# Performance work log

Measured on AMD Instinct MI355X. Metric: run time of the kernel, lower is better.

Reference implementation:

```python
import jax, jax.numpy as jnp
import numpy as np

N, C_S, C_Z, H, D = 512, 384, 128, 16, 24  # c_hidden per head
EPS = 1e-5

def _ln(x, g, b):
    m = jnp.mean(x, axis=-1, keepdims=True)
    v = jnp.mean(jnp.square(x - m), axis=-1, keepdims=True)
    return (x - m) * jax.lax.rsqrt(v + EPS) * g + b

def setup_inputs() -> dict:
    key = jax.random.key(0)
    ks = jax.random.split(key, 12)
    s = lambda fan: 1.0 / np.sqrt(fan)
    return {
        "a": jax.random.normal(ks[0], (1, N, C_S), jnp.float32),
        "z": jax.random.normal(ks[1], (1, N, N, C_Z), jnp.float32),
        "g_a": jnp.ones((C_S,), jnp.float32),
        "b_a": jnp.zeros((C_S,), jnp.float32),
        "g_z": jnp.ones((C_Z,), jnp.float32),
        "b_z": jnp.zeros((C_Z,), jnp.float32),
        "Wz": jax.random.normal(ks[2], (C_Z, H), jnp.float32) * s(C_Z),
        "bz": jnp.zeros((H,), jnp.float32),
        "Wq": jax.random.normal(ks[3], (C_S, H * D), jnp.float32) * s(C_S),
        "Wk": jax.random.normal(ks[4], (C_S, H * D), jnp.float32) * s(C_S),
        "Wv": jax.random.normal(ks[5], (C_S, H * D), jnp.float32) * s(C_S),
        "Wg": jax.random.normal(ks[6], (C_S, H * D), jnp.float32) * s(C_S),
        "bg": jnp.zeros((H * D,), jnp.float32),
        "Wo": jax.random.normal(ks[7], (H * D, C_S), jnp.float32) * s(H * D),
        "bo": jnp.zeros((C_S,), jnp.float32),
    }

def reference(a, z, g_a, b_a, g_z, b_z, Wz, bz, Wq, Wk, Wv, Wg, bg, Wo, bo):
    B = a.shape[0]
    a_n = _ln(a, g_a, b_a)                       # [B,N,C_S]
    z_n = _ln(z, g_z, b_z)                       # [B,N,N,C_Z]
    # linear_z then permute(0,3,1,2): [B,N,N,H] -> [B,H,N,N]
    pair_bias = jnp.einsum('bijc,ch->bhij', z_n, Wz) + bz[None, :, None, None]
    q = (a_n @ Wq).reshape(B, N, H, D) * (1.0 / np.sqrt(D))
    k = (a_n @ Wk).reshape(B, N, H, D)
    v = (a_n @ Wv).reshape(B, N, H, D)
    scores = jnp.einsum('bqhd,bkhd->bhqk', q, k) + pair_bias
    p = jax.nn.softmax(scores, axis=-1)
    o = jnp.einsum('bhqk,bkhd->bqhd', p, v)      # [B,N,H,D]
    g = jax.nn.sigmoid(a_n @ Wg + bg).reshape(B, N, H, D)
    o = (o * g).reshape(B, N, H * D)
    return o @ Wo + bo                            # [B,N,C_S]
```

## Files before the change

kernel.cpp:

```cpp
#include <hip/hip_runtime.h>
#include <math.h>

#define N 512
#define CS 384
#define CZ 128
#define NH 16
#define DH 24
#define HD 384
#define NN (N*N)
#define EPS 1e-5f

#define OFF_AN   0
#define OFF_QT   196608
#define OFF_KT   393216
#define OFF_VT   589824
#define OFF_GT   786432
#define OFF_OG   983040
#define OFF_WZ2  1179648
#define OFF_SH   1181696
#define OFF_BH   1181712
#define OFF_BIAS 1181728

__global__ void prep_kernel(const float* __restrict__ g_z, const float* __restrict__ lnb_z,
                            const float* __restrict__ Wz, const float* __restrict__ bz,
                            float* __restrict__ wz2, float* __restrict__ sh, float* __restrict__ bh) {
    int t = threadIdx.x;
    for (int i = t; i < NH * CZ; i += 256) {
        int h = i >> 7, c = i & (CZ - 1);
        wz2[h * CZ + c] = g_z[c] * Wz[c * NH + h];
    }
    __shared__ float ls[NH][17], lb[NH][17];
    int h = t >> 4, seg = t & 15;
    float s = 0.f, b = 0.f;
    #pragma unroll
    for (int i = 0; i < 8; ++i) {
        int c = seg * 8 + i;
        float w = Wz[c * NH + h];
        s += g_z[c] * w;
        b += lnb_z[c] * w;
    }
    ls[h][seg] = s; lb[h][seg] = b;
    __syncthreads();
    if (t < NH) {
        float ss = 0.f, bb = 0.f;
        #pragma unroll
        for (int i = 0; i < 16; ++i) { ss += ls[t][i]; bb += lb[t][i]; }
        sh[t] = ss;
        bh[t] = bb + bz[t];
    }
}

__global__ void ln_a_kernel(const float* __restrict__ a, const float* __restrict__ g_a,
                            const float* __restrict__ b_a, float* __restrict__ an_out) {
    int r = blockIdx.x, t = threadIdx.x;
    const float* row = a + r * CS;
    float x0 = row[t], x1 = row[t + 128], x2 = row[t + 256];
    float s1 = x0 + x1 + x2;
    float s2 = x0 * x0 + x1 * x1 + x2 * x2;
    #pragma unroll
    for (int m = 1; m < 64; m <<= 1) {
        s1 += __shfl_xor(s1, m, 64);
        s2 += __shfl_xor(s2, m, 64);
    }
    __shared__ float ls1[2], ls2[2];
    if ((t & 63) == 0) { ls1[t >> 6] = s1; ls2[t >> 6] = s2; }
    __syncthreads();
    s1 = ls1[0] + ls1[1];
    s2 = ls2[0] + ls2[1];
    float mu = s1 * (1.f / CS);
    float var = s2 * (1.f / CS) - mu * mu;
    float rs = rsqrtf(var + EPS);
    float* an = an_out + r * CS;
    an[t]       = (x0 - mu) * rs * g_a[t]       + b_a[t];
    an[t + 128] = (x1 - mu) * rs * g_a[t + 128] + b_a[t + 128];
    an[t + 256] = (x2 - mu) * rs * g_a[t + 256] + b_a[t + 256];
}

__global__ void __launch_bounds__(256) qkvg_kernel(const float* __restrict__ Wq, const float* __restrict__ Wk,
                                                   const float* __restrict__ Wv, const float* __restrict__ Wg,
                                                   const float* __restrict__ bg, const float* __restrict__ an,
                                                   float* __restrict__ qt, float* __restrict__ kt,
                                                   float* __restrict__ vt, float* __restrict__ gt) {
    const int lane = threadIdx.x & 63;
    const int w = __builtin_amdgcn_readfirstlane(threadIdx.x >> 6);
    const int strip = blockIdx.x * 4 + w;
    const int n0 = strip * 8;
    const int sel = n0 / HD;
    const int col = n0 % HD;
    const float* Wm = (sel == 0) ? Wq : (sel == 1) ? Wk : (sel == 2) ? Wv : Wg;
    const int m = blockIdx.y * 64 + lane;
    const float* arow = an + m * CS;
    float acc[8];
    #pragma unroll
    for (int j = 0; j < 8; ++j) acc[j] = 0.f;
    for (int kb = 0; kb < CS; kb += 32) {
        float4 av[8];
        #pragma unroll
        for (int i = 0; i < 8; ++i) av[i] = ((const float4*)(arow + kb))[i];
        #pragma unroll
        for (int i = 0; i < 8; ++i) {
            const float* wr = Wm + (kb + i * 4) * HD + col;
            #pragma unroll
            for (int j = 0; j < 8; ++j) {
                acc[j] += av[i].x * wr[j];
                acc[j] += av[i].y * wr[HD + j];
                acc[j] += av[i].z * wr[2 * HD + j];
                acc[j] += av[i].w * wr[3 * HD + j];
            }
        }
    }
    float* dst = (sel == 0) ? qt : (sel == 1) ? kt : (sel == 2) ? vt : gt;
    if (sel == 3) {
        #pragma unroll
        for (int j = 0; j < 8; ++j) acc[j] = 1.f / (1.f + __expf(-(acc[j] + bg[col + j])));
    } else if (sel == 0) {
        #pragma unroll
        for (int j = 0; j < 8; ++j) acc[j] *= 0.20412414523193153f;
    }
    #pragma unroll
    for (int j = 0; j < 8; ++j) {
        int c = col + j;
        int h = c / DH, d = c % DH;
        dst[(h * N + m) * DH + d] = acc[j];
    }
}

__global__ void __launch_bounds__(256) pairbias_kernel(const float* __restrict__ z,
                                                       const float* __restrict__ wz2,
                                                       const float* __restrict__ sh,
                                                       const float* __restrict__ bh,
                                                       float* __restrict__ bias) {
    const int row = blockIdx.x * 256 + threadIdx.x;
    const float* zr = z + (size_t)row * CZ;
    float dots[NH];
    #pragma unroll
    for (int h = 0; h < NH; ++h) dots[h] = 0.f;
    float s1 = 0.f, s2 = 0.f;
    #pragma unroll
    for (int cb = 0; cb < CZ; cb += 32) {
        float4 zv[8];
        #pragma unroll
        for (int i = 0; i < 8; ++i) zv[i] = ((const float4*)(zr + cb))[i];
        #pragma unroll
        for (int i = 0; i < 8; ++i) {
            s1 += zv[i].x + zv[i].y + zv[i].z + zv[i].w;
            s2 += zv[i].x * zv[i].x + zv[i].y * zv[i].y + zv[i].z * zv[i].z + zv[i].w * zv[i].w;
        }
        #pragma unroll
        for (int h = 0; h < NH; ++h) {
            const float* wrow = wz2 + h * CZ + cb;
            float d = dots[h];
            #pragma unroll
            for (int i = 0; i < 8; ++i) {
                d += zv[i].x * wrow[i * 4 + 0];
                d += zv[i].y * wrow[i * 4 + 1];
                d += zv[i].z * wrow[i * 4 + 2];
                d += zv[i].w * wrow[i * 4 + 3];
            }
            dots[h] = d;
        }
    }
    float mu = s1 * (1.f / CZ);
    float var = s2 * (1.f / CZ) - mu * mu;
    float r = rsqrtf(var + EPS);
    #pragma unroll
    for (int h = 0; h < NH; ++h)
        bias[h * NN + row] = r * (dots[h] - mu * sh[h]) + bh[h];
}

__global__ void __launch_bounds__(256) attn_kernel(const float* __restrict__ qt, const float* __restrict__ kt,
                                                   const float* __restrict__ vt, const float* __restrict__ gt,
                                                   const float* __restrict__ bias, float* __restrict__ og) {
    const int lane = threadIdx.x & 63;
    const int w = __builtin_amdgcn_readfirstlane(threadIdx.x >> 6);
    const int qhalf = lane >> 5;
    const int klane = lane & 31;
    const int h = blockIdx.y;
    const int q = blockIdx.x * 8 + w * 2 + qhalf;
    const float* qT = qt + h * N * DH;
    const float* kT = kt + h * N * DH;
    const float* vT = vt + h * N * DH;

    float qv[DH];
    #pragma unroll
    for (int d6 = 0; d6 < 6; ++d6) {
        float4 t4 = ((const float4*)(qT + q * DH))[d6];
        qv[d6 * 4 + 0] = t4.x; qv[d6 * 4 + 1] = t4.y; qv[d6 * 4 + 2] = t4.z; qv[d6 * 4 + 3] = t4.w;
    }
    float sc[16];
    #pragma unroll
    for (int t = 0; t < 16; ++t) {
        const int kk = t * 32 + klane;
        const float4* kr = (const float4*)(kT + kk * DH);
        float4 k0 = kr[0], k1 = kr[1], k2 = kr[2], k3 = kr[3], k4 = kr[4], k5 = kr[5];
        float s = qv[0]*k0.x + qv[1]*k0.y + qv[2]*k0.z + qv[3]*k0.w
                + qv[4]*k1.x + qv[5]*k1.y + qv[6]*k1.z + qv[7]*k1.w
                + qv[8]*k2.x + qv[9]*k2.y + qv[10]*k2.z + qv[11]*k2.w
                + qv[12]*k3.x + qv[13]*k3.y + qv[14]*k3.z + qv[15]*k3.w
                + qv[16]*k4.x + qv[17]*k4.y + qv[18]*k4.z + qv[19]*k4.w
                + qv[20]*k5.x + qv[21]*k5.y + qv[22]*k5.z + qv[23]*k5.w;
        sc[t] = s + bias[h * NN + q * N + kk];
    }
    float mx = sc[0];
    #pragma unroll
    for (int t = 1; t < 16; ++t) mx = fmaxf(mx, sc[t]);
    #pragma unroll
    for (int m = 1; m < 32; m <<= 1) mx = fmaxf(mx, __shfl_xor(mx, m, 64));
    float sum = 0.f;
    #pragma unroll
    for (int t = 0; t < 16; ++t) { sc[t] = __expf(sc[t] - mx); sum += sc[t]; }
    #pragma unroll
    for (int m = 1; m < 32; m <<= 1) sum += __shfl_xor(sum, m, 64);
    float inv = 1.f / sum;
    #pragma unroll
    for (int t = 0; t < 16; ++t) sc[t] *= inv;
    float acc[DH];
    #pragma unroll
    for (int d = 0; d < DH; ++d) acc[d] = 0.f;
    #pragma unroll
    for (int t = 0; t < 16; ++t) {
        const int kk = t * 32 + klane;
        const float4* vr = (const float4*)(vT + kk * DH);
        float4 v0 = vr[0], v1 = vr[1], v2 = vr[2], v3 = vr[3], v4 = vr[4], v5 = vr[5];
        float p = sc[t];
        acc[0] += p*v0.x;  acc[1] += p*v0.y;  acc[2] += p*v0.z;  acc[3] += p*v0.w;
        acc[4] += p*v1.x;  acc[5] += p*v1.y;  acc[6] += p*v1.z;  acc[7] += p*v1.w;
        acc[8] += p*v2.x;  acc[9] += p*v2.y;  acc[10] += p*v2.z; acc[11] += p*v2.w;
        acc[12] += p*v3.x; acc[13] += p*v3.y; acc[14] += p*v3.z; acc[15] += p*v3.w;
        acc[16] += p*v4.x; acc[17] += p*v4.y; acc[18] += p*v4.z; acc[19] += p*v4.w;
        acc[20] += p*v5.x; acc[21] += p*v5.y; acc[22] += p*v5.z; acc[23] += p*v5.w;
    }
    #pragma unroll
    for (int m = 1; m < 32; m <<= 1) {
        #pragma unroll
        for (int d = 0; d < DH; ++d) acc[d] += __shfl_xor(acc[d], m, 64);
    }
    float o = 0.f;
    #pragma unroll
    for (int d = 0; d < DH; ++d) o = (klane == d) ? acc[d] : o;
    if (klane < DH) {
        float g = gt[h * N * DH + q * DH + klane];
        og[q * HD + h * DH + klane] = o * g;
    }
}

__global__ void __launch_bounds__(256) out_gemm_kernel(const float* __restrict__ Wo, const float* __restrict__ bo,
                                                       const float* __restrict__ og, float* __restrict__ out) {
    const int lane = threadIdx.x & 63;
    const int w = __builtin_amdgcn_readfirstlane(threadIdx.x >> 6);
    const int strip = blockIdx.x * 4 + w;
    const int c0 = strip * 4;
    const int m = blockIdx.y * 64 + lane;
    const float* orow = og + m * HD;
    float acc[4];
    #pragma unroll
    for (int j = 0; j < 4; ++j) acc[j] = 0.f;
    for (int kb = 0; kb < HD; kb += 32) {
        float4 av[8];
        #pragma unroll
        for (int i = 0; i < 8; ++i) av[i] = ((const float4*)(orow + kb))[i];
        #pragma unroll
        for (int i = 0; i < 8; ++i) {
            const float* wr = Wo + (kb + i * 4) * CS + c0;
            #pragma unroll
            for (int j = 0; j < 4; ++j) {
                acc[j] += av[i].x * wr[j];
                acc[j] += av[i].y * wr[CS + j];
                acc[j] += av[i].z * wr[2 * CS + j];
                acc[j] += av[i].w * wr[3 * CS + j];
            }
        }
    }
    #pragma unroll
    for (int j = 0; j < 4; ++j) out[m * CS + c0 + j] = acc[j] + bo[c0 + j];
}

extern "C" void kernel_launch(void* const* d_in, const int* in_sizes, int n_in,
                              void* d_out, int out_size, void* d_ws, size_t ws_size,
                              hipStream_t stream) {
    const float* a    = (const float*)d_in[0];
    const float* z    = (const float*)d_in[1];
    const float* g_a  = (const float*)d_in[2];
    const float* b_a  = (const float*)d_in[3];
    const float* g_z  = (const float*)d_in[4];
    const float* b_z  = (const float*)d_in[5];
    const float* Wz   = (const float*)d_in[6];
    const float* bz   = (const float*)d_in[7];
    const float* Wq   = (const float*)d_in[8];
    const float* Wk   = (const float*)d_in[9];
    const float* Wv   = (const float*)d_in[10];
    const float* Wg   = (const float*)d_in[11];
    const float* bg   = (const float*)d_in[12];
    const float* Wo   = (const float*)d_in[13];
    const float* bo   = (const float*)d_in[14];
    float* ws  = (float*)d_ws;
    float* out = (float*)d_out;

    float* an   = ws + OFF_AN;
    float* qt   = ws + OFF_QT;
    float* kt   = ws + OFF_KT;
    float* vt   = ws + OFF_VT;
    float* gt   = ws + OFF_GT;
    float* ogp  = ws + OFF_OG;
    float* wz2  = ws + OFF_WZ2;
    float* shp  = ws + OFF_SH;
    float* bhp  = ws + OFF_BH;
    float* bias = ws + OFF_BIAS;

    hipLaunchKernelGGL(prep_kernel,     dim3(1),      dim3(256), 0, stream, g_z, b_z, Wz, bz, wz2, shp, bhp);
    hipLaunchKernelGGL(ln_a_kernel,     dim3(512),    dim3(128), 0, stream, a, g_a, b_a, an);
    hipLaunchKernelGGL(qkvg_kernel,     dim3(48, 8),  dim3(256), 0, stream, Wq, Wk, Wv, Wg, bg, an, qt, kt, vt, gt);
    hipLaunchKernelGGL(pairbias_kernel, dim3(1024),   dim3(256), 0, stream, z, wz2, shp, bhp, bias);
    hipLaunchKernelGGL(attn_kernel,     dim3(64, 16), dim3(256), 0, stream, qt, kt, vt, gt, bias, ogp);
    hipLaunchKernelGGL(out_gemm_kernel, dim3(24, 8),  dim3(256), 0, stream, Wo, bo, ogp, out);
}
```

Measured before the change: 338.5 us.

## Merge prep/LN and QKVG/pair-bias kernels, narrow GEMM strips for more waves

Result: slower. 362.8 us (+7.2%).

```diff
diff --git a/kernel.cpp b/kernel.cpp
--- a/kernel.cpp
+++ b/kernel.cpp
@@ -21,40 +21,45 @@
 #define OFF_BH   1181712
 #define OFF_BIAS 1181728
 
-__global__ void prep_kernel(const float* __restrict__ g_z, const float* __restrict__ lnb_z,
-                            const float* __restrict__ Wz, const float* __restrict__ bz,
-                            float* __restrict__ wz2, float* __restrict__ sh, float* __restrict__ bh) {
-    int t = threadIdx.x;
-    for (int i = t; i < NH * CZ; i += 256) {
-        int h = i >> 7, c = i & (CZ - 1);
-        wz2[h * CZ + c] = g_z[c] * Wz[c * NH + h];
-    }
+__global__ void __launch_bounds__(256) ln_prep_kernel(const float* __restrict__ a, const float* __restrict__ g_a,
+                                                      const float* __restrict__ b_a, float* __restrict__ an_out,
+                                                      const float* __restrict__ g_z, const float* __restrict__ lnb_z,
+                                                      const float* __restrict__ Wz, const float* __restrict__ bz,
+                                                      float* __restrict__ wz2, float* __restrict__ sh,
+                                                      float* __restrict__ bh) {
     __shared__ float ls[NH][17], lb[NH][17];
-    int h = t >> 4, seg = t & 15;
-    float s = 0.f, b = 0.f;
-    #pragma unroll
-    for (int i = 0; i < 8; ++i) {
-        int c = seg * 8 + i;
-        float w = Wz[c * NH + h];
-        s += g_z[c] * w;
-        b += lnb_z[c] * w;
-    }
-    ls[h][seg] = s; lb[h][seg] = b;
-    __syncthreads();
-    if (t < NH) {
-        float ss = 0.f, bb = 0.f;
-        #pragma unroll
-        for (int i = 0; i < 16; ++i) { ss += ls[t][i]; bb += lb[t][i]; }
-        sh[t] = ss;
-        bh[t] = bb + bz[t];
-    }
-}
-
-__global__ void ln_a_kernel(const float* __restrict__ a, const float* __restrict__ g_a,
-                            const float* __restrict__ b_a, float* __restrict__ an_out) {
-    int r = blockIdx.x, t = threadIdx.x;
+    __shared__ float l1[4], l2[4];
+    const int t = threadIdx.x;
+    if (blockIdx.x == 256) {
+        for (int i = t; i < NH * CZ; i += 256) {
+            int h = i >> 7, c = i & (CZ - 1);
+            wz2[h * CZ + c] = g_z[c] * Wz[c * NH + h];
+        }
+        int h = t >> 4, seg = t & 15;
+        float s = 0.f, b = 0.f;
+        #pragma unroll
+        for (int i = 0; i < 8; ++i) {
+            int c = seg * 8 + i;
+            float w = Wz[c * NH + h];
+            s += g_z[c] * w;
+            b += lnb_z[c] * w;
+        }
+        ls[h][seg] = s; lb[h][seg] = b;
+        __syncthreads();
+        if (t < NH) {
+            float ss = 0.f, bb = 0.f;
+            #pragma unroll
+            for (int i = 0; i < 16; ++i) { ss += ls[t][i]; bb += lb[t][i]; }
+            sh[t] = ss;
+            bh[t] = bb + bz[t];
+        }
+        return;
+    }
+    const int half = t >> 7;
+    const int tr = t & 127;
+    const int r = blockIdx.x * 2 + half;
     const float* row = a + r * CS;
-    float x0 = row[t], x1 = row[t + 128], x2 = row[t + 256];
+    float x0 = row[tr], x1 = row[tr + 128], x2 = row[tr + 256];
     float s1 = x0 + x1 + x2;
     float s2 = x0 * x0 + x1 * x1 + x2 * x2;
     #pragma unroll
@@ -62,110 +67,111 @@
         s1 += __shfl_xor(s1, m, 64);
         s2 += __shfl_xor(s2, m, 64);
     }
-    __shared__ float ls1[2], ls2[2];
-    if ((t & 63) == 0) { ls1[t >> 6] = s1; ls2[t >> 6] = s2; }
+    if ((t & 63) == 0) { l1[t >> 6] = s1; l2[t >> 6] = s2; }
     __syncthreads();
-    s1 = ls1[0] + ls1[1];
-    s2 = ls2[0] + ls2[1];
+    s1 = l1[half * 2] + l1[half * 2 + 1];
+    s2 = l2[half * 2] + l2[half * 2 + 1];
     float mu = s1 * (1.f / CS);
     float var = s2 * (1.f / CS) - mu * mu;
     float rs = rsqrtf(var + EPS);
     float* an = an_out + r * CS;
-    an[t]       = (x0 - mu) * rs * g_a[t]       + b_a[t];
-    an[t + 128] = (x1 - mu) * rs * g_a[t + 128] + b_a[t + 128];
-    an[t + 256] = (x2 - mu) * rs * g_a[t + 256] + b_a[t + 256];
-}
-
-__global__ void __launch_bounds__(256) qkvg_kernel(const float* __restrict__ Wq, const float* __restrict__ Wk,
-                                                   const float* __restrict__ Wv, const float* __restrict__ Wg,
-                                                   const float* __restrict__ bg, const float* __restrict__ an,
-                                                   float* __restrict__ qt, float* __restrict__ kt,
-                                                   float* __restrict__ vt, float* __restrict__ gt) {
-    const int lane = threadIdx.x & 63;
-    const int w = __builtin_amdgcn_readfirstlane(threadIdx.x >> 6);
-    const int strip = blockIdx.x * 4 + w;
-    const int n0 = strip * 8;
-    const int sel = n0 / HD;
-    const int col = n0 % HD;
-    const float* Wm = (sel == 0) ? Wq : (sel == 1) ? Wk : (sel == 2) ? Wv : Wg;
-    const int m = blockIdx.y * 64 + lane;
-    const float* arow = an + m * CS;
-    float acc[8];
-    #pragma unroll
-    for (int j = 0; j < 8; ++j) acc[j] = 0.f;
-    for (int kb = 0; kb < CS; kb += 32) {
-        float4 av[8];
-        #pragma unroll
-        for (int i = 0; i < 8; ++i) av[i] = ((const float4*)(arow + kb))[i];
-        #pragma unroll
-        for (int i = 0; i < 8; ++i) {
-            const float* wr = Wm + (kb + i * 4) * HD + col;
-            #pragma unroll
-            for (int j = 0; j < 8; ++j) {
-                acc[j] += av[i].x * wr[j];
-                acc[j] += av[i].y * wr[HD + j];
-                acc[j] += av[i].z * wr[2 * HD + j];
-                acc[j] += av[i].w * wr[3 * HD + j];
+    an[tr]       = (x0 - mu) * rs * g_a[tr]       + b_a[tr];
+    an[tr + 128] = (x1 - mu) * rs * g_a[tr + 128] + b_a[tr + 128];
+    an[tr + 256] = (x2 - mu) * rs * g_a[tr + 256] + b_a[tr + 256];
+}
+
+__global__ void __launch_bounds__(256) qp_kernel(const float* __restrict__ Wq, const float* __restrict__ Wk,
+                                                 const float* __restrict__ Wv, const float* __restrict__ Wg,
+                                                 const float* __restrict__ bg, const float* __restrict__ an,
+                                                 float* __restrict__ qt, float* __restrict__ kt,
+                                                 float* __restrict__ vt, float* __restrict__ gt,
+                                                 const float* __restrict__ z, const float* __restrict__ wz2,
+                                                 const float* __restrict__ sh, const float* __restrict__ bh,
+                                                 float* __restrict__ bias) {
+    const int b = blockIdx.x;
+    if (b < 768) {
+        const int lane = threadIdx.x & 63;
+        const int w = __builtin_amdgcn_readfirstlane(threadIdx.x >> 6);
+        const int wid = b * 4 + w;
+        const int strip = wid >> 3;
+        const int mb = wid & 7;
+        const int n0 = strip * 4;
+        const int sel = n0 / HD;
+        const int col = n0 % HD;
+        const float* Wm = (sel == 0) ? Wq : (sel == 1) ? Wk : (sel == 2) ? Wv : Wg;
+        const int m = mb * 64 + lane;
+        const float* arow = an + m * CS;
+        float acc[4];
+        #pragma unroll
+        for (int j = 0; j < 4; ++j) acc[j] = 0.f;
+        for (int kb = 0; kb < CS; kb += 32) {
+            float4 av[8];
+            #pragma unroll
+            for (int i = 0; i < 8; ++i) av[i] = ((const float4*)(arow + kb))[i];
+            #pragma unroll
+            for (int i = 0; i < 8; ++i) {
+                const float* wr = Wm + (kb + i * 4) * HD + col;
+                #pragma unroll
+                for (int j = 0; j < 4; ++j) {
+                    acc[j] += av[i].x * wr[j];
+                    acc[j] += av[i].y * wr[HD + j];
+                    acc[j] += av[i].z * wr[2 * HD + j];
+                    acc[j] += av[i].w * wr[3 * HD + j];
+                }
             }
         }
-    }
-    float* dst = (sel == 0) ? qt : (sel == 1) ? kt : (sel == 2) ? vt : gt;
-    if (sel == 3) {
-        #pragma unroll
-        for (int j = 0; j < 8; ++j) acc[j] = 1.f / (1.f + __expf(-(acc[j] + bg[col + j])));
-    } else if (sel == 0) {
-        #pragma unroll
-        for (int j = 0; j < 8; ++j) acc[j] *= 0.20412414523193153f;
-    }
-    #pragma unroll
-    for (int j = 0; j < 8; ++j) {
-        int c = col + j;
-        int h = c / DH, d = c % DH;
-        dst[(h * N + m) * DH + d] = acc[j];
-    }
-}
-
-__global__ void __launch_bounds__(256) pairbias_kernel(const float* __restrict__ z,
-                                                       const float* __restrict__ wz2,
-                                                       const float* __restrict__ sh,
-                                                       const float* __restrict__ bh,
-                                                       float* __restrict__ bias) {
-    const int row = blockIdx.x * 256 + threadIdx.x;
-    const float* zr = z + (size_t)row * CZ;
-    float dots[NH];
-    #pragma unroll
-    for (int h = 0; h < NH; ++h) dots[h] = 0.f;
-    float s1 = 0.f, s2 = 0.f;
-    #pragma unroll
-    for (int cb = 0; cb < CZ; cb += 32) {
-        float4 zv[8];
-        #pragma unroll
-        for (int i = 0; i < 8; ++i) zv[i] = ((const float4*)(zr + cb))[i];
-        #pragma unroll
-        for (int i = 0; i < 8; ++i) {
-            s1 += zv[i].x + zv[i].y + zv[i].z + zv[i].w;
-            s2 += zv[i].x * zv[i].x + zv[i].y * zv[i].y + zv[i].z * zv[i].z + zv[i].w * zv[i].w;
-        }
-        #pragma unroll
-        for (int h = 0; h < NH; ++h) {
-            const float* wrow = wz2 + h * CZ + cb;
-            float d = dots[h];
+        float* dst = (sel == 0) ? qt : (sel == 1) ? kt : (sel == 2) ? vt : gt;
+        if (sel == 3) {
+            #pragma unroll
+            for (int j = 0; j < 4; ++j) acc[j] = 1.f / (1.f + __expf(-(acc[j] + bg[col + j])));
+        } else if (sel == 0) {
+            #pragma unroll
+            for (int j = 0; j < 4; ++j) acc[j] *= 0.20412414523193153f;
+        }
+        #pragma unroll
+        for (int j = 0; j < 4; ++j) {
+            int c = col + j;
+            int h = c / DH, d = c % DH;
+            dst[(h * N + m) * DH + d] = acc[j];
+        }
+    } else {
+        const int row = (b - 768) * 256 + threadIdx.x;
+        const float* zr = z + (size_t)row * CZ;
+        float dots[NH];
+        #pragma unroll
+        for (int h = 0; h < NH; ++h) dots[h] = 0.f;
+        float s1 = 0.f, s2 = 0.f;
+        #pragma unroll
+        for (int cb = 0; cb < CZ; cb += 32) {
+            float4 zv[8];
+            #pragma unroll
+            for (int i = 0; i < 8; ++i) zv[i] = ((const float4*)(zr + cb))[i];
             #pragma unroll
             for (int i = 0; i < 8; ++i) {
-                d += zv[i].x * wrow[i * 4 + 0];
-                d += zv[i].y * wrow[i * 4 + 1];
-                d += zv[i].z * wrow[i * 4 + 2];
-                d += zv[i].w * wrow[i * 4 + 3];
+                s1 += zv[i].x + zv[i].y + zv[i].z + zv[i].w;
+                s2 += zv[i].x * zv[i].x + zv[i].y * zv[i].y + zv[i].z * zv[i].z + zv[i].w * zv[i].w;
             }
-            dots[h] = d;
-        }
-    }
-    float mu = s1 * (1.f / CZ);
-    float var = s2 * (1.f / CZ) - mu * mu;
-    float r = rsqrtf(var + EPS);
-    #pragma unroll
-    for (int h = 0; h < NH; ++h)
-        bias[h * NN + row] = r * (dots[h] - mu * sh[h]) + bh[h];
+            #pragma unroll
+            for (int h = 0; h < NH; ++h) {
+                const float* wrow = wz2 + h * CZ + cb;
+                float d = dots[h];
+                #pragma unroll
+                for (int i = 0; i < 8; ++i) {
+                    d += zv[i].x * wrow[i * 4 + 0];
+                    d += zv[i].y * wrow[i * 4 + 1];
+                    d += zv[i].z * wrow[i * 4 + 2];
+                    d += zv[i].w * wrow[i * 4 + 3];
+                }
+                dots[h] = d;
+            }
+        }
+        float mu = s1 * (1.f / CZ);
+        float var = s2 * (1.f / CZ) - mu * mu;
+        float r = rsqrtf(var + EPS);
+        #pragma unroll
+        for (int h = 0; h < NH; ++h)
+            bias[h * NN + row] = r * (dots[h] - mu * sh[h]) + bh[h];
+    }
 }
 
 __global__ void __launch_bounds__(256) attn_kernel(const float* __restrict__ qt, const float* __restrict__ kt,
@@ -248,13 +254,14 @@
                                                        const float* __restrict__ og, float* __restrict__ out) {
     const int lane = threadIdx.x & 63;
     const int w = __builtin_amdgcn_readfirstlane(threadIdx.x >> 6);
-    const int strip = blockIdx.x * 4 + w;
-    const int c0 = strip * 4;
-    const int m = blockIdx.y * 64 + lane;
+    const int wid = blockIdx.x * 4 + w;
+    const int strip = wid >> 3;
+    const int mb = wid & 7;
+    const int c0 = strip * 2;
+    const int m = mb * 64 + lane;
     const float* orow = og + m * HD;
-    float acc[4];
-    #pragma unroll
-    for (int j = 0; j < 4; ++j) acc[j] = 0.f;
+    float acc[2];
+    acc[0] = 0.f; acc[1] = 0.f;
     for (int kb = 0; kb < HD; kb += 32) {
         float4 av[8];
         #pragma unroll
@@ -263,7 +270,7 @@
         for (int i = 0; i < 8; ++i) {
             const float* wr = Wo + (kb + i * 4) * CS + c0;
             #pragma unroll
-            for (int j = 0; j < 4; ++j) {
+            for (int j = 0; j < 2; ++j) {
                 acc[j] += av[i].x * wr[j];
                 acc[j] += av[i].y * wr[CS + j];
                 acc[j] += av[i].z * wr[2 * CS + j];
@@ -272,7 +279,7 @@
         }
     }
     #pragma unroll
-    for (int j = 0; j < 4; ++j) out[m * CS + c0 + j] = acc[j] + bo[c0 + j];
+    for (int j = 0; j < 2; ++j) out[m * CS + c0 + j] = acc[j] + bo[c0 + j];
 }
 
 extern "C" void kernel_launch(void* const* d_in, const int* in_sizes, int n_in,
@@ -307,10 +314,12 @@
     float* bhp  = ws + OFF_BH;
     float* bias = ws + OFF_BIAS;
 
-    hipLaunchKernelGGL(prep_kernel,     dim3(1),      dim3(256), 0, stream, g_z, b_z, Wz, bz, wz2, shp, bhp);
-    hipLaunchKernelGGL(ln_a_kernel,     dim3(512),    dim3(128), 0, stream, a, g_a, b_a, an);
-    hipLaunchKernelGGL(qkvg_kernel,     dim3(48, 8),  dim3(256), 0, stream, Wq, Wk, Wv, Wg, bg, an, qt, kt, vt, gt);
-    hipLaunchKernelGGL(pairbias_kernel, dim3(1024),   dim3(256), 0, stream, z, wz2, shp, bhp, bias);
-    hipLaunchKernelGGL(attn_kernel,     dim3(64, 16), dim3(256), 0, stream, qt, kt, vt, gt, bias, ogp);
-    hipLaunchKernelGGL(out_gemm_kernel, dim3(24, 8),  dim3(256), 0, stream, Wo, bo, ogp, out);
-}
+    hipLaunchKernelGGL(ln_prep_kernel, dim3(257),    dim3(256), 0, stream,
+                       a, g_a, b_a, an, g_z, b_z, Wz, bz, wz2, shp, bhp);
+    hipLaunchKernelGGL(qp_kernel,      dim3(1792),   dim3(256), 0, stream,
+                       Wq, Wk, Wv, Wg, bg, an, qt, kt, vt, gt, z, wz2, shp, bhp, bias);
+    hipLaunchKernelGGL(attn_kernel,    dim3(64, 16), dim3(256), 0, stream,
+                       qt, kt, vt, gt, bias, ogp);
+    hipLaunchKernelGGL(out_gemm_kernel, dim3(384),   dim3(256), 0, stream,
+                       Wo, bo, ogp, out);
+}
```

## Split pair-bias rows across 16 lanes with shuffle reductions; merge LN and prep kernels

Applied to the files above, without the earlier changes.

Result: slower. 356.4 us (+5.3%).

```diff
diff --git a/kernel.cpp b/kernel.cpp
--- a/kernel.cpp
+++ b/kernel.cpp
@@ -21,40 +21,45 @@
 #define OFF_BH   1181712
 #define OFF_BIAS 1181728
 
-__global__ void prep_kernel(const float* __restrict__ g_z, const float* __restrict__ lnb_z,
-                            const float* __restrict__ Wz, const float* __restrict__ bz,
-                            float* __restrict__ wz2, float* __restrict__ sh, float* __restrict__ bh) {
-    int t = threadIdx.x;
-    for (int i = t; i < NH * CZ; i += 256) {
-        int h = i >> 7, c = i & (CZ - 1);
-        wz2[h * CZ + c] = g_z[c] * Wz[c * NH + h];
-    }
+__global__ void __launch_bounds__(256) ln_prep_kernel(const float* __restrict__ a, const float* __restrict__ g_a,
+                                                      const float* __restrict__ b_a, float* __restrict__ an_out,
+                                                      const float* __restrict__ g_z, const float* __restrict__ lnb_z,
+                                                      const float* __restrict__ Wz, const float* __restrict__ bz,
+                                                      float* __restrict__ wz2, float* __restrict__ sh,
+                                                      float* __restrict__ bh) {
     __shared__ float ls[NH][17], lb[NH][17];
-    int h = t >> 4, seg = t & 15;
-    float s = 0.f, b = 0.f;
-    #pragma unroll
-    for (int i = 0; i < 8; ++i) {
-        int c = seg * 8 + i;
-        float w = Wz[c * NH + h];
-        s += g_z[c] * w;
-        b += lnb_z[c] * w;
-    }
-    ls[h][seg] = s; lb[h][seg] = b;
-    __syncthreads();
-    if (t < NH) {
-        float ss = 0.f, bb = 0.f;
-        #pragma unroll
-        for (int i = 0; i < 16; ++i) { ss += ls[t][i]; bb += lb[t][i]; }
-        sh[t] = ss;
-        bh[t] = bb + bz[t];
-    }
-}
-
-__global__ void ln_a_kernel(const float* __restrict__ a, const float* __restrict__ g_a,
-                            const float* __restrict__ b_a, float* __restrict__ an_out) {
-    int r = blockIdx.x, t = threadIdx.x;
+    __shared__ float l1[4], l2[4];
+    const int t = threadIdx.x;
+    if (blockIdx.x == 256) {
+        for (int i = t; i < NH * CZ; i += 256) {
+            int h = i >> 7, c = i & (CZ - 1);
+            wz2[h * CZ + c] = g_z[c] * Wz[c * NH + h];
+        }
+        int h = t >> 4, seg = t & 15;
+        float s = 0.f, b = 0.f;
+        #pragma unroll
+        for (int i = 0; i < 8; ++i) {
+            int c = seg * 8 + i;
+            float w = Wz[c * NH + h];
+            s += g_z[c] * w;
+            b += lnb_z[c] * w;
+        }
+        ls[h][seg] = s; lb[h][seg] = b;
+        __syncthreads();
+        if (t < NH) {
+            float ss = 0.f, bb = 0.f;
+            #pragma unroll
+            for (int i = 0; i < 16; ++i) { ss += ls[t][i]; bb += lb[t][i]; }
+            sh[t] = ss;
+            bh[t] = bb + bz[t];
+        }
+        return;
+    }
+    const int half = t >> 7;
+    const int tr = t & 127;
+    const int r = blockIdx.x * 2 + half;
     const float* row = a + r * CS;
-    float x0 = row[t], x1 = row[t + 128], x2 = row[t + 256];
+    float x0 = row[tr], x1 = row[tr + 128], x2 = row[tr + 256];
     float s1 = x0 + x1 + x2;
     float s2 = x0 * x0 + x1 * x1 + x2 * x2;
     #pragma unroll
@@ -62,18 +67,17 @@
         s1 += __shfl_xor(s1, m, 64);
         s2 += __shfl_xor(s2, m, 64);
     }
-    __shared__ float ls1[2], ls2[2];
-    if ((t & 63) == 0) { ls1[t >> 6] = s1; ls2[t >> 6] = s2; }
+    if ((t & 63) == 0) { l1[t >> 6] = s1; l2[t >> 6] = s2; }
     __syncthreads();
-    s1 = ls1[0] + ls1[1];
-    s2 = ls2[0] + ls2[1];
+    s1 = l1[half * 2] + l1[half * 2 + 1];
+    s2 = l2[half * 2] + l2[half * 2 + 1];
     float mu = s1 * (1.f / CS);
     float var = s2 * (1.f / CS) - mu * mu;
     float rs = rsqrtf(var + EPS);
     float* an = an_out + r * CS;
-    an[t]       = (x0 - mu) * rs * g_a[t]       + b_a[t];
-    an[t + 128] = (x1 - mu) * rs * g_a[t + 128] + b_a[t + 128];
-    an[t + 256] = (x2 - mu) * rs * g_a[t + 256] + b_a[t + 256];
+    an[tr]       = (x0 - mu) * rs * g_a[tr]       + b_a[tr];
+    an[tr + 128] = (x1 - mu) * rs * g_a[tr + 128] + b_a[tr + 128];
+    an[tr + 256] = (x2 - mu) * rs * g_a[tr + 256] + b_a[tr + 256];
 }
 
 __global__ void __launch_bounds__(256) qkvg_kernel(const float* __restrict__ Wq, const float* __restrict__ Wk,
@@ -130,42 +134,44 @@
                                                        const float* __restrict__ sh,
                                                        const float* __restrict__ bh,
                                                        float* __restrict__ bias) {
-    const int row = blockIdx.x * 256 + threadIdx.x;
-    const float* zr = z + (size_t)row * CZ;
-    float dots[NH];
-    #pragma unroll
-    for (int h = 0; h < NH; ++h) dots[h] = 0.f;
-    float s1 = 0.f, s2 = 0.f;
-    #pragma unroll
-    for (int cb = 0; cb < CZ; cb += 32) {
-        float4 zv[8];
-        #pragma unroll
-        for (int i = 0; i < 8; ++i) zv[i] = ((const float4*)(zr + cb))[i];
-        #pragma unroll
-        for (int i = 0; i < 8; ++i) {
-            s1 += zv[i].x + zv[i].y + zv[i].z + zv[i].w;
-            s2 += zv[i].x * zv[i].x + zv[i].y * zv[i].y + zv[i].z * zv[i].z + zv[i].w * zv[i].w;
-        }
+    const int lane = threadIdx.x & 63;
+    const int w = threadIdx.x >> 6;
+    const int r4 = lane >> 4;
+    const int cl = lane & 15;
+    const int wave_row0 = blockIdx.x * 128 + w * 32;
+    const float shc = sh[cl];
+    const float bhc = bh[cl];
+    for (int g = 0; g < 8; ++g) {
+        const int row = wave_row0 + g * 4 + r4;
+        const float* zr = z + (size_t)row * CZ + cl * 8;
+        float4 z0 = ((const float4*)zr)[0];
+        float4 z1 = ((const float4*)zr)[1];
+        float s1 = z0.x + z0.y + z0.z + z0.w + z1.x + z1.y + z1.z + z1.w;
+        float s2 = z0.x*z0.x + z0.y*z0.y + z0.z*z0.z + z0.w*z0.w
+                 + z1.x*z1.x + z1.y*z1.y + z1.z*z1.z + z1.w*z1.w;
+        float dots[NH];
         #pragma unroll
         for (int h = 0; h < NH; ++h) {
-            const float* wrow = wz2 + h * CZ + cb;
-            float d = dots[h];
+            const float4* wp = (const float4*)(wz2 + h * CZ + cl * 8);
+            float4 w0 = wp[0], w1 = wp[1];
+            dots[h] = z0.x*w0.x + z0.y*w0.y + z0.z*w0.z + z0.w*w0.w
+                    + z1.x*w1.x + z1.y*w1.y + z1.z*w1.z + z1.w*w1.w;
+        }
+        #pragma unroll
+        for (int m = 1; m < 16; m <<= 1) {
+            s1 += __shfl_xor(s1, m, 64);
+            s2 += __shfl_xor(s2, m, 64);
             #pragma unroll
-            for (int i = 0; i < 8; ++i) {
-                d += zv[i].x * wrow[i * 4 + 0];
-                d += zv[i].y * wrow[i * 4 + 1];
-                d += zv[i].z * wrow[i * 4 + 2];
-                d += zv[i].w * wrow[i * 4 + 3];
-            }
-            dots[h] = d;
-        }
-    }
-    float mu = s1 * (1.f / CZ);
-    float var = s2 * (1.f / CZ) - mu * mu;
-    float r = rsqrtf(var + EPS);
-    #pragma unroll
-    for (int h = 0; h < NH; ++h)
-        bias[h * NN + row] = r * (dots[h] - mu * sh[h]) + bh[h];
+            for (int h = 0; h < NH; ++h) dots[h] += __shfl_xor(dots[h], m, 64);
+        }
+        float mu = s1 * (1.f / CZ);
+        float var = s2 * (1.f / CZ) - mu * mu;
+        float rr = rsqrtf(var + EPS);
+        float d = dots[0];
+        #pragma unroll
+        for (int h = 1; h < NH; ++h) d = (cl == h) ? dots[h] : d;
+        bias[cl * NN + row] = rr * (d - mu * shc) + bhc;
+    }
 }
 
 __global__ void __launch_bounds__(256) attn_kernel(const float* __restrict__ qt, const float* __restrict__ kt,
@@ -307,10 +313,14 @@
     float* bhp  = ws + OFF_BH;
     float* bias = ws + OFF_BIAS;
 
-    hipLaunchKernelGGL(prep_kernel,     dim3(1),      dim3(256), 0, stream, g_z, b_z, Wz, bz, wz2, shp, bhp);
-    hipLaunchKernelGGL(ln_a_kernel,     dim3(512),    dim3(128), 0, stream, a, g_a, b_a, an);
-    hipLaunchKernelGGL(qkvg_kernel,     dim3(48, 8),  dim3(256), 0, stream, Wq, Wk, Wv, Wg, bg, an, qt, kt, vt, gt);
-    hipLaunchKernelGGL(pairbias_kernel, dim3(1024),   dim3(256), 0, stream, z, wz2, shp, bhp, bias);
-    hipLaunchKernelGGL(attn_kernel,     dim3(64, 16), dim3(256), 0, stream, qt, kt, vt, gt, bias, ogp);
-    hipLaunchKernelGGL(out_gemm_kernel, dim3(24, 8),  dim3(256), 0, stream, Wo, bo, ogp, out);
-}
+    hipLaunchKernelGGL(ln_prep_kernel, dim3(257),    dim3(256), 0, stream,
+                       a, g_a, b_a, an, g_z, b_z, Wz, bz, wz2, shp, bhp);
+    hipLaunchKernelGGL(qkvg_kernel,    dim3(48, 8),  dim3(256), 0, stream,
+                       Wq, Wk, Wv, Wg, bg, an, qt, kt, vt, gt);
+    hipLaunchKernelGGL(pairbias_kernel, dim3(2048),  dim3(256), 0, stream,
+                       z, wz2, shp, bhp, bias);
+    hipLaunchKernelGGL(attn_kernel,    dim3(64, 16), dim3(256), 0, stream,
+                       qt, kt, vt, gt, bias, ogp);
+    hipLaunchKernelGGL(out_gemm_kernel, dim3(24, 8), dim3(256), 0, stream,
+                       Wo, bo, ogp, out);
+}
```
